# Kernel optimization log

Measured on AMD Instinct MI355X. Metric: run time of the kernel, lower is better.

Reference implementation:

```python
import jax, jax.numpy as jnp
import numpy as np

N, E, D, H, C, HOPS = 50000, 1600000, 128, 4, 32, 3

def spectral_normalize(W, iters=5):
    # power iteration, fixed start vector (deterministic, jit-friendly)
    u = jnp.ones((W.shape[0],), W.dtype) / jnp.sqrt(jnp.float32(W.shape[0]))
    for _ in range(iters):
        v = W.T @ u; v = v / (jnp.linalg.norm(v) + 1e-12)
        u = W @ v;  u = u / (jnp.linalg.norm(u) + 1e-12)
    sigma = u @ (W @ v)
    return W / (sigma + 1e-12)

def layer_norm(x, g, b, eps=1e-5):
    m = jnp.mean(x, -1, keepdims=True)
    v = jnp.mean((x - m) ** 2, -1, keepdims=True)
    return (x - m) * jax.lax.rsqrt(v + eps) * g + b

def edge_softmax(logits, dst):
    # logits: [E, H]; softmax over edges sharing a destination node
    m = jax.ops.segment_max(logits, dst, num_segments=N)
    e = jnp.exp(logits - m[dst])
    s = jax.ops.segment_sum(e, dst, num_segments=N)
    return e / (s[dst] + 1e-16)

def gat_layer(h, src, dst, W, a_s, a_d, bias):
    xh = (h @ W).reshape(N, H, C)                      # [N,H,C]
    al_s = jnp.sum(xh * a_s, -1)                       # [N,H]
    al_d = jnp.sum(xh * a_d, -1)
    logits = jax.nn.leaky_relu(al_s[src] + al_d[dst], 0.2)  # [E,H]
    alpha = edge_softmax(logits, dst)                  # [E,H]
    msg = xh[src] * alpha[..., None]                   # [E,H,C]
    out = jax.ops.segment_sum(msg, dst, num_segments=N)
    return out.reshape(N, H * C) + bias

def ode_block(h, W_ode, b_ode, steps=4):
    # fixed-step RK4 over t in [0,1]; f(h) = gelu(h @ sn(W) + b)
    Wn = spectral_normalize(W_ode)
    f = lambda y: jax.nn.gelu(y @ Wn + b_ode, approximate=False)
    dt = 1.0 / steps
    def step(y, _):
        k1 = f(y); k2 = f(y + 0.5 * dt * k1)
        k3 = f(y + 0.5 * dt * k2); k4 = f(y + dt * k3)
        return y + (dt / 6.0) * (k1 + 2 * k2 + 2 * k3 + k4), None
    y, _ = jax.lax.scan(step, h, None, length=steps)
    return y

def multihop_broadcast(h, src, dst, att):
    deg = jnp.maximum(jax.ops.segment_sum(jnp.ones((E,), h.dtype), dst, num_segments=N), 1.0)
    hops = [h]
    cur = h
    for _ in range(HOPS):
        cur = jax.ops.segment_sum(cur[src], dst, num_segments=N) / deg[:, None]
        hops.append(cur)
    stack = jnp.stack(hops)                            # [HOPS+1, N, D]
    scores = jnp.einsum('knd,d->kn', stack, att)       # [HOPS+1, N]
    w = jax.nn.softmax(scores, axis=0)
    return jnp.einsum('kn,knd->nd', w, stack)

def encoder_fwd(x, edge_index, W_in, b_in, W1, a_src1, a_dst1, b1,
                W2, a_src2, a_dst2, b2, g1, be1, g2, be2, W_ode, b_ode, att):
    src, dst = edge_index[0], edge_index[1]
    h = jax.nn.gelu(x @ spectral_normalize(W_in) + b_in, approximate=False)
    h = layer_norm(jax.nn.gelu(gat_layer(h, src, dst, W1, a_src1, a_dst1, b1), approximate=False), g1, be1)
    h = layer_norm(jax.nn.gelu(gat_layer(h, src, dst, W2, a_src2, a_dst2, b2), approximate=False), g2, be2)
    h = ode_block(h, W_ode, b_ode)
    h = multihop_broadcast(h, src, dst, att)
    return h

def setup_inputs() -> dict:
    key = jax.random.key(0)
    ks = jax.random.split(key, 12)
    s = lambda d: 1.0 / np.sqrt(d)
    return {
        'x': jax.random.normal(ks[0], (N, D), jnp.float32),
        'edge_index': jax.random.randint(ks[1], (2, E), 0, N, jnp.int64),
        'W_in': jax.random.normal(ks[2], (D, D), jnp.float32) * s(D),
        'b_in': jnp.zeros((D,), jnp.float32),
        'W1': jax.random.normal(ks[3], (D, H * C), jnp.float32) * s(D),
        'a_src1': jax.random.normal(ks[4], (H, C), jnp.float32) * s(C),
        'a_dst1': jax.random.normal(ks[5], (H, C), jnp.float32) * s(C),
        'b1': jnp.zeros((H * C,), jnp.float32),
        'W2': jax.random.normal(ks[6], (D, H * C), jnp.float32) * s(D),
        'a_src2': jax.random.normal(ks[7], (H, C), jnp.float32) * s(C),
        'a_dst2': jax.random.normal(ks[8], (H, C), jnp.float32) * s(C),
        'b2': jnp.zeros((H * C,), jnp.float32),
        'g1': jnp.ones((D,), jnp.float32), 'be1': jnp.zeros((D,), jnp.float32),
        'g2': jnp.ones((D,), jnp.float32), 'be2': jnp.zeros((D,), jnp.float32),
        'W_ode': jax.random.normal(ks[9], (D, D), jnp.float32) * s(D),
        'b_ode': jnp.zeros((D,), jnp.float32),
        'att': jax.random.normal(ks[10], (D,), jnp.float32) * s(D),
    }

def reference(x, edge_index, W_in, b_in, W1, a_src1, a_dst1, b1, W2, a_src2, a_dst2, b2,
              g1, be1, g2, be2, W_ode, b_ode, att):
    return encoder_fwd(x, edge_index, W_in, b_in, W1, a_src1, a_dst1, b1,
                       W2, a_src2, a_dst2, b2, g1, be1, g2, be2, W_ode, b_ode, att)
```

## Files before the change

### kernel.cpp

```cpp
#include <hip/hip_runtime.h>
#include <math.h>


typedef __attribute__((ext_vector_type(8))) short bf16x8;
typedef __attribute__((ext_vector_type(4))) float f32x4;

#define BSN 256

__device__ __forceinline__ float gelu_f(float x) {
    return 0.5f * x * (1.0f + erff(x * 0.70710678118654752f));
}
__device__ __forceinline__ unsigned pack_bf16(float a, float b) {
    unsigned ua = __float_as_uint(a), ub = __float_as_uint(b);
    ua += 0x7fffu + ((ua >> 16) & 1u);
    ub += 0x7fffu + ((ub >> 16) & 1u);
    return (ua >> 16) | (ub & 0xffff0000u);
}
__device__ __forceinline__ unsigned short bfbits(float x) {
    unsigned u = __float_as_uint(x);
    u += 0x7fffu + ((u >> 16) & 1u);
    return (unsigned short)(u >> 16);
}
__device__ __forceinline__ float bf_lo(unsigned u) { return __uint_as_float(u << 16); }
__device__ __forceinline__ float bf_hi(unsigned u) { return __uint_as_float(u & 0xffff0000u); }
__device__ __forceinline__ int swz(int byte) { return byte ^ (((byte >> 8) & 15) << 4); }

__launch_bounds__(128, 1)
__global__ void sn_k(const float* __restrict__ Win, const float* __restrict__ Wode,
                     float* __restrict__ WnIn, float* __restrict__ WnOde)
{
    __shared__ float Ws[128 * 128];
    __shared__ float Wt[128 * 128];
    __shared__ float red[128];
    const float* W  = (blockIdx.x == 0) ? Win  : Wode;
    float*       Wn = (blockIdx.x == 0) ? WnIn : WnOde;
    const int t = threadIdx.x;

    for (int i = t * 4; i < 16384; i += 512) {
        float4 v = *(const float4*)&W[i];
        *(float4*)&Ws[i] = v;
        int r = i >> 7, c = i & 127;
        Wt[(c + 0) * 128 + r] = v.x;
        Wt[(c + 1) * 128 + r] = v.y;
        Wt[(c + 2) * 128 + r] = v.z;
        Wt[(c + 3) * 128 + r] = v.w;
    }
    __syncthreads();

    float u = 0.088388347648318447f;
    float v = 0.0f;
    for (int it = 0; it < 5; it++) {
        red[t] = u; __syncthreads();
        float vv = 0.f;
        for (int i = 0; i < 128; i++) vv = fmaf(Ws[i * 128 + t], red[i], vv);
        __syncthreads();
        red[t] = vv * vv; __syncthreads();
        for (int s = 64; s > 0; s >>= 1) { if (t < s) red[t] += red[t + s]; __syncthreads(); }
        float nv = sqrtf(red[0]) + 1e-12f;
        v = vv / nv;
        __syncthreads();
        red[t] = v; __syncthreads();
        float uu = 0.f;
        for (int i = 0; i < 128; i++) uu = fmaf(Wt[i * 128 + t], red[i], uu);
        __syncthreads();
        red[t] = uu * uu; __syncthreads();
        for (int s = 64; s > 0; s >>= 1) { if (t < s) red[t] += red[t + s]; __syncthreads(); }
        float nu = sqrtf(red[0]) + 1e-12f;
        u = uu / nu;
        __syncthreads();
    }
    red[t] = v; __syncthreads();
    float wv = 0.f;
    for (int i = 0; i < 128; i++) wv = fmaf(Wt[i * 128 + t], red[i], wv);
    __syncthreads();
    red[t] = u * wv; __syncthreads();
    for (int s = 64; s > 0; s >>= 1) { if (t < s) red[t] += red[t + s]; __syncthreads(); }
    float inv = 1.0f / (red[0] + 1e-12f);
    __syncthreads();
    for (int i = t * 4; i < 16384; i += 512) {
        float4 w = *(const float4*)&Ws[i];
        w.x *= inv; w.y *= inv; w.z *= inv; w.w *= inv;
        *(float4*)&Wn[i] = w;
    }
}

__global__ void hist_k(const int* __restrict__ dst, int* __restrict__ deg, int E, int N)
{
    int e = blockIdx.x * blockDim.x + threadIdx.x;
    if (e < E) {
        int d = dst[e];
        d = (d < 0) ? 0 : (d >= N ? N - 1 : d);
        atomicAdd(&deg[d], 1);
    }
}

__launch_bounds__(1024, 1)
__global__ void scan_k(const int* __restrict__ deg, int* __restrict__ offs, int n)
{
    __shared__ int part[1024];
    const int t = threadIdx.x;
    const int chunk = (n + 1023) >> 10;
    int lo = t * chunk; if (lo > n) lo = n;
    int hi = lo + chunk; if (hi > n) hi = n;
    int s = 0;
    for (int i = lo; i < hi; i++) s += deg[i];
    part[t] = s; __syncthreads();
    for (int d = 1; d < 1024; d <<= 1) {
        int v = (t >= d) ? part[t - d] : 0;
        __syncthreads();
        part[t] += v;
        __syncthreads();
    }
    int run = (t == 0) ? 0 : part[t - 1];
    for (int i = lo; i < hi; i++) { offs[i] = run; run += deg[i]; }
    if (t == 1023) offs[n] = run;
}

__global__ void binit_k(const int* __restrict__ offs, int* __restrict__ bcur, int N, int nb)
{
    int b = blockIdx.x * blockDim.x + threadIdx.x;
    if (b < nb) {
        int n = b * BSN; if (n > N) n = N;
        bcur[b] = offs[n];
    }
}

__launch_bounds__(256, 2)
__global__ void scatA_k(const int* __restrict__ src, const int* __restrict__ dst,
                        int* __restrict__ bcur, uint2* __restrict__ pairbuf, int E, int N)
{
    __shared__ int cnt[256];
    __shared__ int sc[256];
    __shared__ int ebase[256];
    __shared__ int delta[256];
    __shared__ uint2 pr[4096];
    __shared__ unsigned char bid[4096];
    const int t = threadIdx.x;
    const int e0 = blockIdx.x * 4096;

    int s[16], d[16], rk[16], bb[16];
    cnt[t] = 0;
    __syncthreads();
#pragma unroll
    for (int i = 0; i < 16; i++) {
        int e = e0 + i * 256 + t;
        if (e < E) {
            int dd = dst[e]; dd = (dd < 0) ? 0 : (dd >= N ? N - 1 : dd);
            int ss = src[e]; ss = (ss < 0) ? 0 : (ss >= N ? N - 1 : ss);
            s[i] = ss; d[i] = dd; bb[i] = dd >> 8;
            rk[i] = atomicAdd(&cnt[bb[i]], 1);
        } else bb[i] = -1;
    }
    __syncthreads();
    sc[t] = cnt[t]; __syncthreads();
    for (int st = 1; st < 256; st <<= 1) {
        int v = (t >= st) ? sc[t - st] : 0;
        __syncthreads();
        sc[t] += v;
        __syncthreads();
    }
    int excl = sc[t] - cnt[t];
    int gbase = (cnt[t] > 0) ? atomicAdd(&bcur[t], cnt[t]) : 0;
    ebase[t] = excl;
    delta[t] = gbase - excl;
    __syncthreads();
#pragma unroll
    for (int i = 0; i < 16; i++) {
        if (bb[i] >= 0) {
            int slot = ebase[bb[i]] + rk[i];
            pr[slot] = make_uint2((unsigned)s[i], (unsigned)d[i]);
            bid[slot] = (unsigned char)bb[i];
        }
    }
    __syncthreads();
    const int total = sc[255];
    for (int i2 = t; i2 < total; i2 += 256) {
        int b = bid[i2];
        pairbuf[delta[b] + i2] = pr[i2];
    }
}

__launch_bounds__(256, 4)
__global__ void scatB_k(const uint2* __restrict__ pairbuf, const int* __restrict__ offs,
                        int* __restrict__ col, int N)
{
    __shared__ int cur[BSN];
    const int b = blockIdx.x;
    const int n0 = b * BSN;
    const int t = threadIdx.x;
    int nn = N - n0; if (nn > BSN) nn = BSN;
    if (t < nn) cur[t] = offs[n0 + t];
    __syncthreads();
    const int es = offs[n0], ee = offs[n0 + nn];
    for (int e = es + t; e < ee; e += 256) {
        uint2 p = pairbuf[e];
        int pos = atomicAdd(&cur[(int)p.y - n0], 1);
        col[pos] = (int)p.x;
    }
}

__launch_bounds__(256, 2)
__global__ void gemm_mfma_k(const float* __restrict__ in, const float* __restrict__ W,
                            const float* __restrict__ bias, float* __restrict__ out_f32,
                            unsigned short* __restrict__ out_bf, int nrows, int mode,
                            const float* __restrict__ a_s, const float* __restrict__ a_d,
                            float* __restrict__ als, float* __restrict__ ald)
{
    __shared__ unsigned short Wt[128 * 128];
    __shared__ unsigned short As[128 * 128];
    const int t = threadIdx.x;
    const int w = t >> 6, lane = t & 63;
    const int cl = lane & 15, lg = lane >> 4;
    const int r0 = blockIdx.x * 128;

    for (int i = t; i < 16384; i += 256) {
        int k = i >> 7, c = i & 127;
        *(unsigned short*)((char*)Wt + swz((c << 8) + (k << 1))) = bfbits(W[i]);
    }
    for (int i2 = t; i2 < 4096; i2 += 256) {
        int r = i2 >> 5, k0 = (i2 & 31) * 4;
        int rc = r0 + r; if (rc > nrows - 1) rc = nrows - 1;
        float4 v = *(const float4*)&in[(size_t)rc * 128 + k0];
        *(uint2*)((char*)As + swz((r << 8) + (k0 << 1))) =
            make_uint2(pack_bf16(v.x, v.y), pack_bf16(v.z, v.w));
    }
    __syncthreads();

    bf16x8 af[2][4];
#pragma unroll
    for (int rt = 0; rt < 2; rt++)
#pragma unroll
        for (int ks = 0; ks < 4; ks++)
            af[rt][ks] = *(const bf16x8*)((char*)As +
                           swz((w * 32 + rt * 16 + cl) * 256 + ks * 64 + lg * 16));

    f32x4 acc[2][8];
#pragma unroll
    for (int rt = 0; rt < 2; rt++)
#pragma unroll
        for (int n = 0; n < 8; n++) acc[rt][n] = (f32x4){0.f, 0.f, 0.f, 0.f};

#pragma unroll
    for (int n = 0; n < 8; n++) {
#pragma unroll
        for (int ks = 0; ks < 4; ks++) {
            bf16x8 bf = *(const bf16x8*)((char*)Wt +
                          swz((n * 16 + cl) * 256 + ks * 64 + lg * 16));
            acc[0][n] = __builtin_amdgcn_mfma_f32_16x16x32_bf16(af[0][ks], bf, acc[0][n], 0, 0, 0);
            acc[1][n] = __builtin_amdgcn_mfma_f32_16x16x32_bf16(af[1][ks], bf, acc[1][n], 0, 0, 0);
        }
    }

    if (mode == 0) {
        float asv[4][2], adv[4][2];
#pragma unroll
        for (int h = 0; h < 4; h++) {
            asv[h][0] = a_s[h * 32 + cl];      asv[h][1] = a_s[h * 32 + 16 + cl];
            adv[h][0] = a_d[h * 32 + cl];      adv[h][1] = a_d[h * 32 + 16 + cl];
        }
#pragma unroll
        for (int rt = 0; rt < 2; rt++) {
#pragma unroll
            for (int q = 0; q < 4; q++) {
                int row = r0 + w * 32 + rt * 16 + lg * 4 + q;
                float sh[4], dh[4];
#pragma unroll
                for (int h = 0; h < 4; h++) {
                    sh[h] = acc[rt][2 * h][q] * asv[h][0] + acc[rt][2 * h + 1][q] * asv[h][1];
                    dh[h] = acc[rt][2 * h][q] * adv[h][0] + acc[rt][2 * h + 1][q] * adv[h][1];
                }
#pragma unroll
                for (int mk = 1; mk < 16; mk <<= 1) {
#pragma unroll
                    for (int h = 0; h < 4; h++) {
                        sh[h] += __shfl_xor(sh[h], mk);
                        dh[h] += __shfl_xor(dh[h], mk);
                    }
                }
                if (cl == 0 && row < nrows) {
#pragma unroll
                    for (int h = 0; h < 4; h++) {
                        als[(size_t)row * 4 + h] = sh[h];
                        ald[(size_t)row * 4 + h] = dh[h];
                    }
                }
            }
#pragma unroll
            for (int q = 0; q < 4; q++) {
                int row = r0 + w * 32 + rt * 16 + lg * 4 + q;
                if (row < nrows) {
#pragma unroll
                    for (int n = 0; n < 8; n++)
                        out_bf[(size_t)row * 128 + n * 16 + cl] = bfbits(acc[rt][n][q]);
                }
            }
        }
    } else {
        float bc[8];
#pragma unroll
        for (int n = 0; n < 8; n++) bc[n] = bias[n * 16 + cl];
#pragma unroll
        for (int rt = 0; rt < 2; rt++)
#pragma unroll
            for (int q = 0; q < 4; q++) {
                int row = r0 + w * 32 + rt * 16 + lg * 4 + q;
                if (row < nrows) {
#pragma unroll
                    for (int n = 0; n < 8; n++)
                        out_f32[(size_t)row * 128 + n * 16 + cl] =
                            gelu_f(acc[rt][n][q] + bc[n]);
                }
            }
    }
}

__launch_bounds__(256)
__global__ void gat_agg2_k(const unsigned* __restrict__ xhbf, const float* __restrict__ als,
                           const float* __restrict__ ald, const int* __restrict__ col,
                           const int* __restrict__ offs, const float* __restrict__ bias,
                           const float* __restrict__ g, const float* __restrict__ be,
                           float* __restrict__ hout, int nnodes)
{
    __shared__ float alph[4][64][4];
    __shared__ int   scol[4][64];
    const int w = threadIdx.x >> 6;
    const int n = blockIdx.x * 4 + w;
    if (n >= nnodes) return;
    const int lane = threadIdx.x & 63;
    const int e0 = offs[n], e1 = offs[n + 1];
    const float4 aldv = *(const float4*)&ald[(size_t)n * 4];

    float m0 = -1e30f, m1 = -1e30f, m2 = -1e30f, m3 = -1e30f;
    float s0 = 0.f, s1 = 0.f, s2 = 0.f, s3 = 0.f;
    for (int i = e0 + lane; i < e1; i += 64) {
        int sv = col[i];
        float4 av = *(const float4*)&als[(size_t)sv * 4];
        float l0 = av.x + aldv.x; l0 = l0 > 0.f ? l0 : 0.2f * l0;
        float l1 = av.y + aldv.y; l1 = l1 > 0.f ? l1 : 0.2f * l1;
        float l2 = av.z + aldv.z; l2 = l2 > 0.f ? l2 : 0.2f * l2;
        float l3 = av.w + aldv.w; l3 = l3 > 0.f ? l3 : 0.2f * l3;
        float M;
        M = fmaxf(m0, l0); s0 = s0 * __expf(m0 - M) + __expf(l0 - M); m0 = M;
        M = fmaxf(m1, l1); s1 = s1 * __expf(m1 - M) + __expf(l1 - M); m1 = M;
        M = fmaxf(m2, l2); s2 = s2 * __expf(m2 - M) + __expf(l2 - M); m2 = M;
        M = fmaxf(m3, l3); s3 = s3 * __expf(m3 - M) + __expf(l3 - M); m3 = M;
    }
#pragma unroll
    for (int mk = 1; mk < 64; mk <<= 1) {
        float mo, so, M;
        mo = __shfl_xor(m0, mk); so = __shfl_xor(s0, mk);
        M = fmaxf(m0, mo); s0 = s0 * __expf(m0 - M) + so * __expf(mo - M); m0 = M;
        mo = __shfl_xor(m1, mk); so = __shfl_xor(s1, mk);
        M = fmaxf(m1, mo); s1 = s1 * __expf(m1 - M) + so * __expf(mo - M); m1 = M;
        mo = __shfl_xor(m2, mk); so = __shfl_xor(s2, mk);
        M = fmaxf(m2, mo); s2 = s2 * __expf(m2 - M) + so * __expf(mo - M); m2 = M;
        mo = __shfl_xor(m3, mk); so = __shfl_xor(s3, mk);
        M = fmaxf(m3, mo); s3 = s3 * __expf(m3 - M) + so * __expf(mo - M); m3 = M;
    }
    const float i0 = 1.f / (s0 + 1e-16f), i1 = 1.f / (s1 + 1e-16f);
    const float i2 = 1.f / (s2 + 1e-16f), i3 = 1.f / (s3 + 1e-16f);

    const int hh = lane >> 4;
    float ax = 0.f, ay = 0.f;
    for (int base = e0; base < e1; base += 64) {
        int idx = base + lane;
        if (idx < e1) {
            int sv = col[idx];
            float4 av = *(const float4*)&als[(size_t)sv * 4];
            float l0 = av.x + aldv.x; l0 = l0 > 0.f ? l0 : 0.2f * l0;
            float l1 = av.y + aldv.y; l1 = l1 > 0.f ? l1 : 0.2f * l1;
            float l2 = av.z + aldv.z; l2 = l2 > 0.f ? l2 : 0.2f * l2;
            float l3 = av.w + aldv.w; l3 = l3 > 0.f ? l3 : 0.2f * l3;
            float4 a4;
            a4.x = __expf(l0 - m0) * i0;
            a4.y = __expf(l1 - m1) * i1;
            a4.z = __expf(l2 - m2) * i2;
            a4.w = __expf(l3 - m3) * i3;
            *(float4*)&alph[w][lane][0] = a4;
            scol[w][lane] = sv;
        }
        int cnt = e1 - base; if (cnt > 64) cnt = 64;
#pragma unroll 4
        for (int j = 0; j < cnt; j++) {
            int sj = scol[w][j];
            float aj = alph[w][j][hh];
            unsigned u = xhbf[(size_t)sj * 64 + lane];
            ax = fmaf(aj, bf_lo(u), ax);
            ay = fmaf(aj, bf_hi(u), ay);
        }
    }

    const int c0 = lane * 2;
    float v0 = gelu_f(ax + bias[c0]);
    float v1 = gelu_f(ay + bias[c0 + 1]);
    float sum = v0 + v1;
#pragma unroll
    for (int mk = 32; mk >= 1; mk >>= 1) sum += __shfl_xor(sum, mk);
    float mean = sum * (1.0f / 128.0f);
    float d0 = v0 - mean, d1 = v1 - mean;
    float vs = d0 * d0 + d1 * d1;
#pragma unroll
    for (int mk = 32; mk >= 1; mk >>= 1) vs += __shfl_xor(vs, mk);
    float rstd = rsqrtf(vs * (1.0f / 128.0f) + 1e-5f);
    size_t b = (size_t)n * 128 + c0;
    hout[b]     = d0 * rstd * g[c0] + be[c0];
    hout[b + 1] = d1 * rstd * g[c0 + 1] + be[c0 + 1];
}

__launch_bounds__(256, 4)
__global__ void ode_mfma_k(const float* __restrict__ yin, const float* __restrict__ Wn,
                           const float* __restrict__ bias, unsigned short* __restrict__ ybf,
                           int nrows, int nchunks)
{
    __shared__ unsigned short Wt[128 * 128];
    __shared__ unsigned short tl[2][16 * 128];
    const int t = threadIdx.x;
    const int w = t >> 6, lane = t & 63;
    const int pair = w >> 1, hf = w & 1;
    const int cl = lane & 15, lg = lane >> 4;

    for (int i = t; i < 16384; i += 256) {
        int k = i >> 7, c = i & 127;
        *(unsigned short*)((char*)Wt + swz((c << 8) + (k << 1))) = bfbits(Wn[i]);
    }

    float bcol[4];
#pragma unroll
    for (int n = 0; n < 4; n++) bcol[n] = bias[(hf * 4 + n) * 16 + cl];

    const float dt = 0.25f;
    char* tbase = (char*)&tl[pair][0];

    int chunk = blockIdx.x * 2 + pair;
    if (chunk > nchunks - 1) chunk = nchunks - 1;
    const int r0 = chunk * 16;

    for (int i2 = hf * 64 + lane; i2 < 512; i2 += 128) {
        int r = i2 >> 5, k0 = (i2 & 31) * 4;
        int rc = r0 + r; if (rc > nrows - 1) rc = nrows - 1;
        float4 v = *(const float4*)&yin[(size_t)rc * 128 + k0];
        *(uint2*)(tbase + swz(r * 256 + k0 * 2)) =
            make_uint2(pack_bf16(v.x, v.y), pack_bf16(v.z, v.w));
    }
    float yv[4][4], av[4][4];
#pragma unroll
    for (int q = 0; q < 4; q++) {
        int rc = r0 + lg * 4 + q; if (rc > nrows - 1) rc = nrows - 1;
        const float* rp = &yin[(size_t)rc * 128 + hf * 64 + cl];
#pragma unroll
        for (int n = 0; n < 4; n++) { yv[n][q] = rp[n * 16]; av[n][q] = yv[n][q]; }
    }
    __syncthreads();

#pragma unroll 1
    for (int step = 0; step < 4; step++) {
#pragma unroll 1
        for (int st = 0; st < 4; st++) {
            const float ca = (st == 0 || st == 3) ? dt / 6.f : dt / 3.f;
            const float ct = (st < 2) ? dt * 0.5f : dt;
            const bool last = (st == 3);
            bf16x8 af[4];
#pragma unroll
            for (int ks = 0; ks < 4; ks++)
                af[ks] = *(const bf16x8*)(tbase + swz(cl * 256 + ks * 64 + lg * 16));
            f32x4 acc[4];
#pragma unroll
            for (int n = 0; n < 4; n++) {
                acc[n] = (f32x4){0.f, 0.f, 0.f, 0.f};
#pragma unroll
                for (int ks = 0; ks < 4; ks++) {
                    bf16x8 bf = *(const bf16x8*)((char*)Wt +
                                  swz(((hf * 4 + n) * 16 + cl) * 256 + ks * 64 + lg * 16));
                    acc[n] = __builtin_amdgcn_mfma_f32_16x16x32_bf16(af[ks], bf, acc[n], 0, 0, 0);
                }
            }
            __syncthreads();
#pragma unroll
            for (int n = 0; n < 4; n++) {
#pragma unroll
                for (int q = 0; q < 4; q++) {
                    float kk = gelu_f(acc[n][q] + bcol[n]);
                    av[n][q] = fmaf(ca, kk, av[n][q]);
                    float tn;
                    if (last) { yv[n][q] = av[n][q]; tn = av[n][q]; }
                    else      { tn = fmaf(ct, kk, yv[n][q]); }
                    int rr = lg * 4 + q;
                    *(unsigned short*)(tbase +
                        swz(rr * 256 + ((hf * 4 + n) * 16 + cl) * 2)) = bfbits(tn);
                }
            }
            __syncthreads();
        }
    }
#pragma unroll
    for (int q = 0; q < 4; q++) {
        int rg = r0 + lg * 4 + q;
        if (rg < nrows) {
#pragma unroll
            for (int n = 0; n < 4; n++)
                ybf[(size_t)rg * 128 + hf * 64 + n * 16 + cl] = bfbits(av[n][q]);
        }
    }
}

__launch_bounds__(256)
__global__ void hop_k(const unsigned* __restrict__ cur, const int* __restrict__ col,
                      const int* __restrict__ offs, const int* __restrict__ deg,
                      unsigned* __restrict__ outbf, int nnodes)
{
    __shared__ int scol[4][64];
    const int w = threadIdx.x >> 6;
    const int n = blockIdx.x * 4 + w;
    if (n >= nnodes) return;
    const int lane = threadIdx.x & 63;
    const int e0 = offs[n], e1 = offs[n + 1];
    float ax = 0.f, ay = 0.f;
    for (int base = e0; base < e1; base += 64) {
        int idx = base + lane;
        if (idx < e1) scol[w][lane] = col[idx];
        int cnt = e1 - base; if (cnt > 64) cnt = 64;
#pragma unroll 4
        for (int j = 0; j < cnt; j++) {
            int sj = scol[w][j];
            unsigned u = cur[(size_t)sj * 64 + lane];
            ax += bf_lo(u); ay += bf_hi(u);
        }
    }
    float dg = fmaxf((float)deg[n], 1.0f);
    outbf[(size_t)n * 64 + lane] = pack_bf16(ax / dg, ay / dg);
}

__launch_bounds__(256)
__global__ void final2_k(const unsigned* __restrict__ s0b, const unsigned* __restrict__ s1b,
                         const unsigned* __restrict__ s2b, const unsigned* __restrict__ s3b,
                         const float* __restrict__ att, float* __restrict__ outp, int nnodes)
{
    const int n = blockIdx.x * 4 + (threadIdx.x >> 6);
    if (n >= nnodes) return;
    const int lane = threadIdx.x & 63;
    size_t b = (size_t)n * 64 + lane;
    float2 a = *(const float2*)&att[lane * 2];
    unsigned u0 = s0b[b], u1 = s1b[b], u2 = s2b[b], u3 = s3b[b];
    float p0 = bf_lo(u0) * a.x + bf_hi(u0) * a.y;
    float p1 = bf_lo(u1) * a.x + bf_hi(u1) * a.y;
    float p2 = bf_lo(u2) * a.x + bf_hi(u2) * a.y;
    float p3 = bf_lo(u3) * a.x + bf_hi(u3) * a.y;
#pragma unroll
    for (int mk = 32; mk >= 1; mk >>= 1) {
        p0 += __shfl_xor(p0, mk); p1 += __shfl_xor(p1, mk);
        p2 += __shfl_xor(p2, mk); p3 += __shfl_xor(p3, mk);
    }
    float mm = fmaxf(fmaxf(p0, p1), fmaxf(p2, p3));
    float e0 = __expf(p0 - mm), e1 = __expf(p1 - mm), e2 = __expf(p2 - mm), e3 = __expf(p3 - mm);
    float inv = 1.0f / (e0 + e1 + e2 + e3);
    float w0 = e0 * inv, w1 = e1 * inv, w2 = e2 * inv, w3 = e3 * inv;
    float ox = w0 * bf_lo(u0) + w1 * bf_lo(u1) + w2 * bf_lo(u2) + w3 * bf_lo(u3);
    float oy = w0 * bf_hi(u0) + w1 * bf_hi(u1) + w2 * bf_hi(u2) + w3 * bf_hi(u3);
    *(float2*)&outp[(size_t)n * 128 + lane * 2] = make_float2(ox, oy);
}

extern "C" void kernel_launch(void* const* d_in, const int* in_sizes, int n_in,
                              void* d_out, int out_size, void* d_ws, size_t ws_size,
                              hipStream_t stream)
{
    const float* x     = (const float*)d_in[0];
    const int*   ei    = (const int*)d_in[1];
    const float* W_in  = (const float*)d_in[2];
    const float* b_in  = (const float*)d_in[3];
    const float* W1    = (const float*)d_in[4];
    const float* a_s1  = (const float*)d_in[5];
    const float* a_d1  = (const float*)d_in[6];
    const float* b1    = (const float*)d_in[7];
    const float* W2    = (const float*)d_in[8];
    const float* a_s2  = (const float*)d_in[9];
    const float* a_d2  = (const float*)d_in[10];
    const float* b2    = (const float*)d_in[11];
    const float* g1    = (const float*)d_in[12];
    const float* be1   = (const float*)d_in[13];
    const float* g2    = (const float*)d_in[14];
    const float* be2   = (const float*)d_in[15];
    const float* W_ode = (const float*)d_in[16];
    const float* b_ode = (const float*)d_in[17];
    const float* att   = (const float*)d_in[18];

    const int N = in_sizes[0] / 128;
    const int E = in_sizes[1] / 2;
    const int* srcv = ei;
    const int* dstv = ei + E;
    const int nb = (N + BSN - 1) / BSN;

    char* wsb = (char*)d_ws;
    size_t off = 0;
    auto alloc = [&](size_t bytes) -> void* {
        void* p = wsb + off;
        off = (off + bytes + 511) & ~(size_t)511;
        return p;
    };
    float*    WnIn   = (float*)alloc(65536);
    float*    WnOde  = (float*)alloc(65536);
    float*    als    = (float*)alloc((size_t)N * 4 * 4);
    float*    ald    = (float*)alloc((size_t)N * 4 * 4);
    int*      deg    = (int*)alloc((size_t)N * 4);
    int*      bcur   = (int*)alloc((size_t)(nb + 1) * 4);
    int*      offs   = (int*)alloc((size_t)(N + 1) * 4);
    int*      col    = (int*)alloc((size_t)E * 4);
    float*    B0     = (float*)alloc((size_t)N * 128 * 4);
    unsigned* xhbf   = (unsigned*)alloc((size_t)N * 64 * 4);
    unsigned* ybf    = (unsigned*)alloc((size_t)N * 64 * 4);
    unsigned* h2bf   = (unsigned*)alloc((size_t)N * 64 * 4);
    unsigned* h3bf   = (unsigned*)alloc((size_t)N * 64 * 4);
    uint2*    pairbuf = (uint2*)ybf;

    (void)hipMemsetAsync(deg, 0, (size_t)N * 4, stream);

    sn_k<<<2, 128, 0, stream>>>(W_in, W_ode, WnIn, WnOde);
    hist_k<<<(E + 255) / 256, 256, 0, stream>>>(dstv, deg, E, N);
    scan_k<<<1, 1024, 0, stream>>>(deg, offs, N);
    binit_k<<<(nb + 255) / 256, 256, 0, stream>>>(offs, bcur, N, nb);
    scatA_k<<<(E + 4095) / 4096, 256, 0, stream>>>(srcv, dstv, bcur, pairbuf, E, N);
    scatB_k<<<nb, 256, 0, stream>>>(pairbuf, offs, col, N);

    const int gblocks = (N + 127) / 128;
    const int ablocks = (N + 3) / 4;

    gemm_mfma_k<<<gblocks, 256, 0, stream>>>(x, WnIn, b_in, B0, nullptr, N, 1,
        nullptr, nullptr, nullptr, nullptr);

    gemm_mfma_k<<<gblocks, 256, 0, stream>>>(B0, W1, nullptr, nullptr,
        (unsigned short*)xhbf, N, 0, a_s1, a_d1, als, ald);
    gat_agg2_k<<<ablocks, 256, 0, stream>>>(xhbf, als, ald, col, offs, b1, g1, be1, B0, N);

    gemm_mfma_k<<<gblocks, 256, 0, stream>>>(B0, W2, nullptr, nullptr,
        (unsigned short*)xhbf, N, 0, a_s2, a_d2, als, ald);
    gat_agg2_k<<<ablocks, 256, 0, stream>>>(xhbf, als, ald, col, offs, b2, g2, be2, B0, N);

    const int nchunks = (N + 15) / 16;
    const int oblocks = (nchunks + 1) / 2;
    ode_mfma_k<<<oblocks, 256, 0, stream>>>(B0, WnOde, b_ode, (unsigned short*)ybf, N, nchunks);

    hop_k<<<ablocks, 256, 0, stream>>>(ybf,  col, offs, deg, xhbf, N);
    hop_k<<<ablocks, 256, 0, stream>>>(xhbf, col, offs, deg, h2bf, N);
    hop_k<<<ablocks, 256, 0, stream>>>(h2bf, col, offs, deg, h3bf, N);
    final2_k<<<ablocks, 256, 0, stream>>>(ybf, xhbf, h2bf, h3bf, att, (float*)d_out, N);
}
```

Measured before the change: 681.7 us.

## Use 32-lane groups per node in GAT/hop aggregation and fast tanh GELU in ODE

The gather-aggregation kernels (GAT and multihop) now assign a 32-thread half-wavefront per destination node instead of a full 64-lane wave. Each lane loads 8 bytes (4 bf16 features), which doubles the nodes per block and halves the per-node serial edge loop overhead and shuffle depth for low-degree nodes. Separately, the ODE kernel swaps the exact erf GELU for a tanh-approximation GELU built on exp, cutting transcendental cost at some accuracy risk. Launch sizes are adjusted accordingly, with final2_k keeping its 4-nodes-per-block grid.

Result: no change. 675.7 us (-0.9%).

```diff
diff --git a/kernel.cpp b/kernel.cpp
--- a/kernel.cpp
+++ b/kernel.cpp
@@ -9,6 +9,11 @@
 
 __device__ __forceinline__ float gelu_f(float x) {
     return 0.5f * x * (1.0f + erff(x * 0.70710678118654752f));
+}
+__device__ __forceinline__ float gelu_fast(float x) {
+    float y = 0.7978845608028654f * fmaf(0.044715f * x, x * x, x);
+    float e = __expf(-2.0f * y);
+    return x / (1.0f + e);
 }
 __device__ __forceinline__ unsigned pack_bf16(float a, float b) {
     unsigned ua = __float_as_uint(a), ub = __float_as_uint(b);
@@ -321,18 +326,18 @@
                            const float* __restrict__ g, const float* __restrict__ be,
                            float* __restrict__ hout, int nnodes)
 {
-    __shared__ float alph[4][64][4];
-    __shared__ int   scol[4][64];
-    const int w = threadIdx.x >> 6;
-    const int n = blockIdx.x * 4 + w;
+    __shared__ float alph[8][32][4];
+    __shared__ int   scol[8][32];
+    const int gq = threadIdx.x >> 5;
+    const int n = blockIdx.x * 8 + gq;
     if (n >= nnodes) return;
-    const int lane = threadIdx.x & 63;
+    const int l = threadIdx.x & 31;
     const int e0 = offs[n], e1 = offs[n + 1];
     const float4 aldv = *(const float4*)&ald[(size_t)n * 4];
 
     float m0 = -1e30f, m1 = -1e30f, m2 = -1e30f, m3 = -1e30f;
     float s0 = 0.f, s1 = 0.f, s2 = 0.f, s3 = 0.f;
-    for (int i = e0 + lane; i < e1; i += 64) {
+    for (int i = e0 + l; i < e1; i += 32) {
         int sv = col[i];
         float4 av = *(const float4*)&als[(size_t)sv * 4];
         float l0 = av.x + aldv.x; l0 = l0 > 0.f ? l0 : 0.2f * l0;
@@ -346,7 +351,7 @@
         M = fmaxf(m3, l3); s3 = s3 * __expf(m3 - M) + __expf(l3 - M); m3 = M;
     }
 #pragma unroll
-    for (int mk = 1; mk < 64; mk <<= 1) {
+    for (int mk = 1; mk < 32; mk <<= 1) {
         float mo, so, M;
         mo = __shfl_xor(m0, mk); so = __shfl_xor(s0, mk);
         M = fmaxf(m0, mo); s0 = s0 * __expf(m0 - M) + so * __expf(mo - M); m0 = M;
@@ -360,10 +365,10 @@
     const float i0 = 1.f / (s0 + 1e-16f), i1 = 1.f / (s1 + 1e-16f);
     const float i2 = 1.f / (s2 + 1e-16f), i3 = 1.f / (s3 + 1e-16f);
 
-    const int hh = lane >> 4;
-    float ax = 0.f, ay = 0.f;
-    for (int base = e0; base < e1; base += 64) {
-        int idx = base + lane;
+    const int hh = l >> 3;
+    float a0 = 0.f, a1 = 0.f, a2 = 0.f, a3 = 0.f;
+    for (int base = e0; base < e1; base += 32) {
+        int idx = base + l;
         if (idx < e1) {
             int sv = col[idx];
             float4 av = *(const float4*)&als[(size_t)sv * 4];
@@ -376,35 +381,45 @@
             a4.y = __expf(l1 - m1) * i1;
             a4.z = __expf(l2 - m2) * i2;
             a4.w = __expf(l3 - m3) * i3;
-            *(float4*)&alph[w][lane][0] = a4;
-            scol[w][lane] = sv;
-        }
-        int cnt = e1 - base; if (cnt > 64) cnt = 64;
+            *(float4*)&alph[gq][l][0] = a4;
+            scol[gq][l] = sv;
+        }
+        int cnt = e1 - base; if (cnt > 32) cnt = 32;
 #pragma unroll 4
         for (int j = 0; j < cnt; j++) {
-            int sj = scol[w][j];
-            float aj = alph[w][j][hh];
-            unsigned u = xhbf[(size_t)sj * 64 + lane];
-            ax = fmaf(aj, bf_lo(u), ax);
-            ay = fmaf(aj, bf_hi(u), ay);
-        }
-    }
-
-    const int c0 = lane * 2;
-    float v0 = gelu_f(ax + bias[c0]);
-    float v1 = gelu_f(ay + bias[c0 + 1]);
-    float sum = v0 + v1;
-#pragma unroll
-    for (int mk = 32; mk >= 1; mk >>= 1) sum += __shfl_xor(sum, mk);
+            int sj = scol[gq][j];
+            float aj = alph[gq][j][hh];
+            uint2 u = *(const uint2*)&xhbf[(size_t)sj * 64 + l * 2];
+            a0 = fmaf(aj, bf_lo(u.x), a0);
+            a1 = fmaf(aj, bf_hi(u.x), a1);
+            a2 = fmaf(aj, bf_lo(u.y), a2);
+            a3 = fmaf(aj, bf_hi(u.y), a3);
+        }
+    }
+
+    const int c0 = l * 4;
+    float4 bv = *(const float4*)&bias[c0];
+    float v0 = gelu_f(a0 + bv.x);
+    float v1 = gelu_f(a1 + bv.y);
+    float v2 = gelu_f(a2 + bv.z);
+    float v3 = gelu_f(a3 + bv.w);
+    float sum = v0 + v1 + v2 + v3;
+#pragma unroll
+    for (int mk = 1; mk < 32; mk <<= 1) sum += __shfl_xor(sum, mk);
     float mean = sum * (1.0f / 128.0f);
-    float d0 = v0 - mean, d1 = v1 - mean;
-    float vs = d0 * d0 + d1 * d1;
-#pragma unroll
-    for (int mk = 32; mk >= 1; mk >>= 1) vs += __shfl_xor(vs, mk);
+    float d0 = v0 - mean, d1 = v1 - mean, d2 = v2 - mean, d3 = v3 - mean;
+    float vs = d0 * d0 + d1 * d1 + d2 * d2 + d3 * d3;
+#pragma unroll
+    for (int mk = 1; mk < 32; mk <<= 1) vs += __shfl_xor(vs, mk);
     float rstd = rsqrtf(vs * (1.0f / 128.0f) + 1e-5f);
-    size_t b = (size_t)n * 128 + c0;
-    hout[b]     = d0 * rstd * g[c0] + be[c0];
-    hout[b + 1] = d1 * rstd * g[c0 + 1] + be[c0 + 1];
+    float4 gv = *(const float4*)&g[c0];
+    float4 ev = *(const float4*)&be[c0];
+    float4 o;
+    o.x = d0 * rstd * gv.x + ev.x;
+    o.y = d1 * rstd * gv.y + ev.y;
+    o.z = d2 * rstd * gv.z + ev.z;
+    o.w = d3 * rstd * gv.w + ev.w;
+    *(float4*)&hout[(size_t)n * 128 + c0] = o;
 }
 
 __launch_bounds__(256, 4)
@@ -479,7 +494,7 @@
             for (int n = 0; n < 4; n++) {
 #pragma unroll
                 for (int q = 0; q < 4; q++) {
-                    float kk = gelu_f(acc[n][q] + bcol[n]);
+                    float kk = gelu_fast(acc[n][q] + bcol[n]);
                     av[n][q] = fmaf(ca, kk, av[n][q]);
                     float tn;
                     if (last) { yv[n][q] = av[n][q]; tn = av[n][q]; }
@@ -508,26 +523,28 @@
                       const int* __restrict__ offs, const int* __restrict__ deg,
                       unsigned* __restrict__ outbf, int nnodes)
 {
-    __shared__ int scol[4][64];
-    const int w = threadIdx.x >> 6;
-    const int n = blockIdx.x * 4 + w;
+    __shared__ int scol[8][32];
+    const int gq = threadIdx.x >> 5;
+    const int n = blockIdx.x * 8 + gq;
     if (n >= nnodes) return;
-    const int lane = threadIdx.x & 63;
+    const int l = threadIdx.x & 31;
     const int e0 = offs[n], e1 = offs[n + 1];
-    float ax = 0.f, ay = 0.f;
-    for (int base = e0; base < e1; base += 64) {
-        int idx = base + lane;
-        if (idx < e1) scol[w][lane] = col[idx];
-        int cnt = e1 - base; if (cnt > 64) cnt = 64;
+    float a0 = 0.f, a1 = 0.f, a2 = 0.f, a3 = 0.f;
+    for (int base = e0; base < e1; base += 32) {
+        int idx = base + l;
+        if (idx < e1) scol[gq][l] = col[idx];
+        int cnt = e1 - base; if (cnt > 32) cnt = 32;
 #pragma unroll 4
         for (int j = 0; j < cnt; j++) {
-            int sj = scol[w][j];
-            unsigned u = cur[(size_t)sj * 64 + lane];
-            ax += bf_lo(u); ay += bf_hi(u);
-        }
-    }
-    float dg = fmaxf((float)deg[n], 1.0f);
-    outbf[(size_t)n * 64 + lane] = pack_bf16(ax / dg, ay / dg);
+            int sj = scol[gq][j];
+            uint2 u = *(const uint2*)&cur[(size_t)sj * 64 + l * 2];
+            a0 += bf_lo(u.x); a1 += bf_hi(u.x);
+            a2 += bf_lo(u.y); a3 += bf_hi(u.y);
+        }
+    }
+    float inv = 1.0f / fmaxf((float)deg[n], 1.0f);
+    *(uint2*)&outbf[(size_t)n * 64 + l * 2] =
+        make_uint2(pack_bf16(a0 * inv, a1 * inv), pack_bf16(a2 * inv, a3 * inv));
 }
 
 __launch_bounds__(256)
@@ -621,7 +638,8 @@
     scatB_k<<<nb, 256, 0, stream>>>(pairbuf, offs, col, N);
 
     const int gblocks = (N + 127) / 128;
-    const int ablocks = (N + 3) / 4;
+    const int ablocks = (N + 7) / 8;
+    const int fblocks = (N + 3) / 4;
 
     gemm_mfma_k<<<gblocks, 256, 0, stream>>>(x, WnIn, b_in, B0, nullptr, N, 1,
         nullptr, nullptr, nullptr, nullptr);
@@ -641,5 +659,5 @@
     hop_k<<<ablocks, 256, 0, stream>>>(ybf,  col, offs, deg, xhbf, N);
     hop_k<<<ablocks, 256, 0, stream>>>(xhbf, col, offs, deg, h2bf, N);
     hop_k<<<ablocks, 256, 0, stream>>>(h2bf, col, offs, deg, h3bf, N);
-    final2_k<<<ablocks, 256, 0, stream>>>(ybf, xhbf, h2bf, h3bf, att, (float*)d_out, N);
-}
+    final2_k<<<fblocks, 256, 0, stream>>>(ybf, xhbf, h2bf, h3bf, att, (float*)d_out, N);
+}
```
